# Kernel tuning notes

Hardware: AMD Instinct MI355X
Metric: run time of the kernel (lower is better)

## Reference

```python
import jax, jax.numpy as jnp
from jax import lax
import numpy as np

HIDDEN = 64
E = 2.0        # SigmaLayer E
E_INFTY = 0.5  # SigmaLayer E_infty


def _glorot(key, shape):
    fan_in, fan_out = shape
    lim = np.sqrt(6.0 / (fan_in + fan_out)).astype(np.float32)
    return jax.random.uniform(key, shape, jnp.float32, -lim, lim)


def setup_inputs() -> dict:
    key = jax.random.key(0)
    ks = jax.random.split(key, 7)
    B, T = 2048, 1024
    x = jax.random.uniform(ks[0], (B, T, 2), jnp.float32)  # [:, :, 0]=eps, [:, :, 1]=dt (>0)
    W1 = _glorot(ks[1], (2, HIDDEN))
    b1 = jnp.zeros((HIDDEN,), jnp.float32)
    W2 = _glorot(ks[2], (HIDDEN, HIDDEN))
    b2 = jnp.zeros((HIDDEN,), jnp.float32)
    W3 = _glorot(ks[3], (HIDDEN, 1))
    b3 = jnp.zeros((1,), jnp.float32)
    return {"x": x, "W1": W1, "b1": b1, "W2": W2, "b2": b2, "W3": W3, "b3": b3}


def reference(x, W1, b1, W2, b2, W3, b3):
    # x: [B, T, 2] -> sigma: [B, T, 1]
    def step(gamma, xt):  # gamma: [B,1], xt: [B,2]
        eps_n = xt[:, :1]
        dt_n = xt[:, 1:2]
        h = jnp.concatenate([eps_n, gamma], axis=-1)      # [B,2]
        h = jnp.tanh(h @ W1 + b1)                         # [B,H]
        h = jnp.tanh(h @ W2 + b2)                         # [B,H]
        gamma_dot = h @ W3 + b3                           # [B,1]
        gamma_new = gamma + dt_n * gamma_dot              # explicit Euler
        return gamma_new, gamma_new

    B = x.shape[0]
    g0 = jnp.zeros((B, 1), x.dtype)
    _, gammas = lax.scan(step, g0, jnp.swapaxes(x, 0, 1))  # [T,B,1]
    gamma = jnp.swapaxes(gammas, 0, 1)                     # [B,T,1]
    eps = x[:, :, :1]
    sigma = E_INFTY * eps + E * (eps - gamma)
    return sigma
```

## Files before the change

### kernel.cpp

```cpp
#include <hip/hip_runtime.h>


typedef float f2 __attribute__((ext_vector_type(2)));
typedef float f4 __attribute__((ext_vector_type(4)));

__device__ __forceinline__ float tanh_fast(float x) {
    float e = __builtin_amdgcn_exp2f(x * 2.885390081777927f);
    float r = __builtin_amdgcn_rcpf(e + 1.0f);
    return fmaf(-2.0f, r, 1.0f);
}

template<int CTRL>
__device__ __forceinline__ float dpp_add(float v) {
    int m = __builtin_amdgcn_update_dpp(0, __float_as_int(v), CTRL, 0xF, 0xF, true);
    return v + __int_as_float(m);
}

__device__ __forceinline__ float quad_sum(float v) {
    v = dpp_add<0xB1>(v);
    v = dpp_add<0x4E>(v);
    return v;
}

__device__ __forceinline__ float wave_sum_bcast(float v) {
    v = dpp_add<0xB1>(v);
    v = dpp_add<0x4E>(v);
    v = dpp_add<0x141>(v);
    v = dpp_add<0x140>(v);
    v = dpp_add<0x142>(v);
    v = dpp_add<0x143>(v);
    return __int_as_float(__builtin_amdgcn_readlane(__float_as_int(v), 63));
}

__device__ __forceinline__ float rl(float v, int k) {
    return __int_as_float(__builtin_amdgcn_readlane(__float_as_int(v), k));
}

__global__ __attribute__((amdgpu_flat_work_group_size(256, 256),
                          amdgpu_waves_per_eu(2, 2)))
void maxwell_scan_kernel(
    const float* __restrict__ x,  const float* __restrict__ W1,
    const float* __restrict__ b1, const float* __restrict__ W2,
    const float* __restrict__ b2, const float* __restrict__ W3,
    const float* __restrict__ b3, float* __restrict__ out)
{
    __shared__ __align__(16) float lds_h1[4][64];
    const int lane = threadIdx.x & 63;
    const int warp = threadIdx.x >> 6;
    const int b    = (blockIdx.x << 2) + warp;

    const int o = lane >> 2;
    const int k = lane & 3;
    const int jsel = o + 16 * k;

    const float w1_0 = W1[lane];
    const float w1_1 = W1[64 + lane];
    const float b1j  = b1[lane];
    const float b2s  = b2[jsel];
    const float w3s  = W3[jsel];
    const float b3s  = b3[0];

    f2 w2r[4][8];
#pragma unroll
    for (int m = 0; m < 4; ++m) {
#pragma unroll
        for (int p = 0; p < 8; ++p) {
            const int i0 = 16 * k + 2 * p;
            const int j  = o + 16 * m;
            w2r[m][p] = (f2){ W2[i0 * 64 + j], W2[(i0 + 1) * 64 + j] };
        }
    }

    float* h1s = lds_h1[warp];
    const f4* hv = (const f4*)h1s + (k << 2);

    const f2* __restrict__ xrow = (const f2*)(x) + (size_t)b * 1024;
    float*    __restrict__ orow = out + (size_t)b * 1024;

    float gamma = 0.0f;
    f2 vx = xrow[lane];

    for (int c = 0; c < 16; ++c) {
        f2 vx_next = vx;
        if (c < 15) vx_next = xrow[(c + 1) * 64 + lane];
        float vsig = 0.0f;

        for (int s = 0; s < 8; ++s) {
            const int k0 = s * 8;
            float pk[8], dtk[8], sg[8];
#pragma unroll
            for (int t = 0; t < 8; ++t) {
                const float e = rl(vx.x, k0 + t);
                dtk[t] = rl(vx.y, k0 + t);
                pk[t]  = fmaf(e, w1_0, b1j);
                sg[t]  = 2.5f * e;
            }

            asm volatile("" : "+v"(w2r[0][0]), "+v"(w2r[0][1]), "+v"(w2r[0][2]), "+v"(w2r[0][3]),
                              "+v"(w2r[0][4]), "+v"(w2r[0][5]), "+v"(w2r[0][6]), "+v"(w2r[0][7]),
                              "+v"(w2r[1][0]), "+v"(w2r[1][1]), "+v"(w2r[1][2]), "+v"(w2r[1][3]),
                              "+v"(w2r[1][4]), "+v"(w2r[1][5]), "+v"(w2r[1][6]), "+v"(w2r[1][7]));
            asm volatile("" : "+v"(w2r[2][0]), "+v"(w2r[2][1]), "+v"(w2r[2][2]), "+v"(w2r[2][3]),
                              "+v"(w2r[2][4]), "+v"(w2r[2][5]), "+v"(w2r[2][6]), "+v"(w2r[2][7]),
                              "+v"(w2r[3][0]), "+v"(w2r[3][1]), "+v"(w2r[3][2]), "+v"(w2r[3][3]),
                              "+v"(w2r[3][4]), "+v"(w2r[3][5]), "+v"(w2r[3][6]), "+v"(w2r[3][7]));

#pragma unroll
            for (int t = 0; t < 8; ++t) {
                const float h1 = tanh_fast(fmaf(gamma, w1_1, pk[t]));
                h1s[lane] = h1;
                __builtin_amdgcn_wave_barrier();

                f2 a0 = {0.f, 0.f}, a1 = {0.f, 0.f}, a2 = {0.f, 0.f}, a3 = {0.f, 0.f};
#pragma unroll
                for (int q = 0; q < 4; ++q) {
                    const f4 h4 = hv[q];
                    const f2 hlo = (f2){h4.x, h4.y};
                    const f2 hhi = (f2){h4.z, h4.w};
                    a0 += hlo * w2r[0][2 * q];  a0 += hhi * w2r[0][2 * q + 1];
                    a1 += hlo * w2r[1][2 * q];  a1 += hhi * w2r[1][2 * q + 1];
                    a2 += hlo * w2r[2][2 * q];  a2 += hhi * w2r[2][2 * q + 1];
                    a3 += hlo * w2r[3][2 * q];  a3 += hhi * w2r[3][2 * q + 1];
                }
                __builtin_amdgcn_wave_barrier();

                float s0 = quad_sum(a0.x + a0.y);
                float s1 = quad_sum(a1.x + a1.y);
                float s2 = quad_sum(a2.x + a2.y);
                float s3 = quad_sum(a3.x + a3.y);
                const float t01 = (k & 1) ? s1 : s0;
                const float t23 = (k & 1) ? s3 : s2;
                const float pre = (k & 2) ? t23 : t01;
                const float h2 = tanh_fast(pre + b2s);

                const float gdot = wave_sum_bcast(h2 * w3s) + b3s;
                gamma = fmaf(dtk[t], gdot, gamma);

                const float sig = fmaf(-2.0f, gamma, sg[t]);
                vsig = (lane == k0 + t) ? sig : vsig;
            }
        }
        orow[c * 64 + lane] = vsig;
        vx = vx_next;
    }
}

extern "C" void kernel_launch(void* const* d_in, const int* in_sizes, int n_in,
                              void* d_out, int out_size, void* d_ws, size_t ws_size,
                              hipStream_t stream) {
    const float* x  = (const float*)d_in[0];
    const float* W1 = (const float*)d_in[1];
    const float* b1 = (const float*)d_in[2];
    const float* W2 = (const float*)d_in[3];
    const float* b2 = (const float*)d_in[4];
    const float* W3 = (const float*)d_in[5];
    const float* b3 = (const float*)d_in[6];
    float* out = (float*)d_out;
    (void)in_sizes; (void)n_in; (void)d_ws; (void)ws_size; (void)out_size;

    maxwell_scan_kernel<<<512, 256, 0, stream>>>(x, W1, b1, W2, b2, W3, b3, out);
}
```

Measured before the change: 420.9 us.

## Use fp16 dot2 with ds_bpermute for hidden layer, fold tanh affine terms

Replaces the LDS store/load exchange of h1 with DPP plus ds_bpermute of packed fp16 pairs, and computes the 64x64 layer with v_dot2 fp16 instructions. The affine part of tanh (1 - 2r) is folded into prescaled weights and biases, so each tanh reduces to exp and rcp. The goal is to shorten the per-timestep serial dependency chain and halve the FMA count. The cost is fp16 precision on h1 and W2 inside a 1024-step recurrence, which may drift from the reference.

```diff
diff --git a/kernel.cpp b/kernel.cpp
--- a/kernel.cpp
+++ b/kernel.cpp
@@ -2,13 +2,9 @@
 
 
 typedef float f2 __attribute__((ext_vector_type(2)));
-typedef float f4 __attribute__((ext_vector_type(4)));
+typedef _Float16 h2v __attribute__((ext_vector_type(2)));
 
-__device__ __forceinline__ float tanh_fast(float x) {
-    float e = __builtin_amdgcn_exp2f(x * 2.885390081777927f);
-    float r = __builtin_amdgcn_rcpf(e + 1.0f);
-    return fmaf(-2.0f, r, 1.0f);
-}
+#define TANH_C 2.885390081777927f
 
 template<int CTRL>
 __device__ __forceinline__ float dpp_add(float v) {
@@ -44,7 +40,6 @@
     const float* __restrict__ b2, const float* __restrict__ W3,
     const float* __restrict__ b3, float* __restrict__ out)
 {
-    __shared__ __align__(16) float lds_h1[4][64];
     const int lane = threadIdx.x & 63;
     const int warp = threadIdx.x >> 6;
     const int b    = (blockIdx.x << 2) + warp;
@@ -56,23 +51,32 @@
     const float w1_0 = W1[lane];
     const float w1_1 = W1[64 + lane];
     const float b1j  = b1[lane];
-    const float b2s  = b2[jsel];
-    const float w3s  = W3[jsel];
-    const float b3s  = b3[0];
 
-    f2 w2r[4][8];
+    const float w3p = -2.0f * W3[jsel];
+    float sW3 = 0.0f;
+    for (int j = 0; j < 64; ++j) sW3 += W3[j];
+    const float b3p = b3[0] + sW3;
+
+    int   w2h[4][8];
+    float b2q[4];
 #pragma unroll
     for (int m = 0; m < 4; ++m) {
+        const int j = o + 16 * m;
+        float cs = 0.0f;
+        for (int i = 0; i < 64; ++i) cs += (float)(_Float16)W2[i * 64 + j];
+        b2q[m] = 0.25f * (b2[j] + cs);
 #pragma unroll
         for (int p = 0; p < 8; ++p) {
             const int i0 = 16 * k + 2 * p;
-            const int j  = o + 16 * m;
-            w2r[m][p] = (f2){ W2[i0 * 64 + j], W2[(i0 + 1) * 64 + j] };
+            h2v pp = { (_Float16)(-2.0f * W2[i0 * 64 + j]),
+                       (_Float16)(-2.0f * W2[(i0 + 1) * 64 + j]) };
+            w2h[m][p] = __builtin_bit_cast(int, pp);
         }
     }
 
-    float* h1s = lds_h1[warp];
-    const f4* hv = (const f4*)h1s + (k << 2);
+    int baddr[8];
+#pragma unroll
+    for (int p = 0; p < 8; ++p) baddr[p] = (16 * k + 2 * p) << 2;
 
     const f2* __restrict__ xrow = (const f2*)(x) + (size_t)b * 1024;
     float*    __restrict__ orow = out + (size_t)b * 1024;
@@ -87,54 +91,78 @@
 
         for (int s = 0; s < 8; ++s) {
             const int k0 = s * 8;
-            float pk[8], dtk[8], sg[8];
+            float pk[8], dtk[8], sg[8], db3[8];
 #pragma unroll
             for (int t = 0; t < 8; ++t) {
                 const float e = rl(vx.x, k0 + t);
                 dtk[t] = rl(vx.y, k0 + t);
                 pk[t]  = fmaf(e, w1_0, b1j);
                 sg[t]  = 2.5f * e;
+                db3[t] = dtk[t] * b3p;
             }
 
-            asm volatile("" : "+v"(w2r[0][0]), "+v"(w2r[0][1]), "+v"(w2r[0][2]), "+v"(w2r[0][3]),
-                              "+v"(w2r[0][4]), "+v"(w2r[0][5]), "+v"(w2r[0][6]), "+v"(w2r[0][7]),
-                              "+v"(w2r[1][0]), "+v"(w2r[1][1]), "+v"(w2r[1][2]), "+v"(w2r[1][3]),
-                              "+v"(w2r[1][4]), "+v"(w2r[1][5]), "+v"(w2r[1][6]), "+v"(w2r[1][7]));
-            asm volatile("" : "+v"(w2r[2][0]), "+v"(w2r[2][1]), "+v"(w2r[2][2]), "+v"(w2r[2][3]),
-                              "+v"(w2r[2][4]), "+v"(w2r[2][5]), "+v"(w2r[2][6]), "+v"(w2r[2][7]),
-                              "+v"(w2r[3][0]), "+v"(w2r[3][1]), "+v"(w2r[3][2]), "+v"(w2r[3][3]),
-                              "+v"(w2r[3][4]), "+v"(w2r[3][5]), "+v"(w2r[3][6]), "+v"(w2r[3][7]));
+            asm volatile("" : "+v"(w2h[0][0]), "+v"(w2h[0][1]), "+v"(w2h[0][2]), "+v"(w2h[0][3]),
+                              "+v"(w2h[0][4]), "+v"(w2h[0][5]), "+v"(w2h[0][6]), "+v"(w2h[0][7]),
+                              "+v"(w2h[1][0]), "+v"(w2h[1][1]), "+v"(w2h[1][2]), "+v"(w2h[1][3]),
+                              "+v"(w2h[1][4]), "+v"(w2h[1][5]), "+v"(w2h[1][6]), "+v"(w2h[1][7]));
+            asm volatile("" : "+v"(w2h[2][0]), "+v"(w2h[2][1]), "+v"(w2h[2][2]), "+v"(w2h[2][3]),
+                              "+v"(w2h[2][4]), "+v"(w2h[2][5]), "+v"(w2h[2][6]), "+v"(w2h[2][7]),
+                              "+v"(w2h[3][0]), "+v"(w2h[3][1]), "+v"(w2h[3][2]), "+v"(w2h[3][3]),
+                              "+v"(w2h[3][4]), "+v"(w2h[3][5]), "+v"(w2h[3][6]), "+v"(w2h[3][7]));
 
 #pragma unroll
             for (int t = 0; t < 8; ++t) {
-                const float h1 = tanh_fast(fmaf(gamma, w1_1, pk[t]));
-                h1s[lane] = h1;
-                __builtin_amdgcn_wave_barrier();
+                const float a  = fmaf(gamma, w1_1, pk[t]);
+                const float ea = __builtin_amdgcn_exp2f(a * TANH_C);
+                const float r  = __builtin_amdgcn_rcpf(ea + 1.0f);
 
-                f2 a0 = {0.f, 0.f}, a1 = {0.f, 0.f}, a2 = {0.f, 0.f}, a3 = {0.f, 0.f};
+                const int nb = __builtin_amdgcn_update_dpp(
+                    0, __float_as_int(r), 0x101, 0xF, 0xF, true);
+                const int packd = __builtin_bit_cast(
+                    int, __builtin_amdgcn_cvt_pkrtz(r, __int_as_float(nb)));
+
+                int w0 = __builtin_amdgcn_ds_bpermute(baddr[0], packd);
+                int w1 = __builtin_amdgcn_ds_bpermute(baddr[1], packd);
+                int w2 = __builtin_amdgcn_ds_bpermute(baddr[2], packd);
+                int w3 = __builtin_amdgcn_ds_bpermute(baddr[3], packd);
+                int w4 = __builtin_amdgcn_ds_bpermute(baddr[4], packd);
+                int w5 = __builtin_amdgcn_ds_bpermute(baddr[5], packd);
+                int w6 = __builtin_amdgcn_ds_bpermute(baddr[6], packd);
+                int w7 = __builtin_amdgcn_ds_bpermute(baddr[7], packd);
+
+                const float gpre = gamma + db3[t];
+
+                float zacc[4];
 #pragma unroll
-                for (int q = 0; q < 4; ++q) {
-                    const f4 h4 = hv[q];
-                    const f2 hlo = (f2){h4.x, h4.y};
-                    const f2 hhi = (f2){h4.z, h4.w};
-                    a0 += hlo * w2r[0][2 * q];  a0 += hhi * w2r[0][2 * q + 1];
-                    a1 += hlo * w2r[1][2 * q];  a1 += hhi * w2r[1][2 * q + 1];
-                    a2 += hlo * w2r[2][2 * q];  a2 += hhi * w2r[2][2 * q + 1];
-                    a3 += hlo * w2r[3][2 * q];  a3 += hhi * w2r[3][2 * q + 1];
+                for (int m = 0; m < 4; ++m) {
+                    float aA = b2q[m], aB = 0.0f;
+                    aA = __builtin_amdgcn_fdot2(__builtin_bit_cast(h2v, w2h[m][0]),
+                                                __builtin_bit_cast(h2v, w0), aA, false);
+                    aB = __builtin_amdgcn_fdot2(__builtin_bit_cast(h2v, w2h[m][4]),
+                                                __builtin_bit_cast(h2v, w4), aB, false);
+                    aA = __builtin_amdgcn_fdot2(__builtin_bit_cast(h2v, w2h[m][1]),
+                                                __builtin_bit_cast(h2v, w1), aA, false);
+                    aB = __builtin_amdgcn_fdot2(__builtin_bit_cast(h2v, w2h[m][5]),
+                                                __builtin_bit_cast(h2v, w5), aB, false);
+                    aA = __builtin_amdgcn_fdot2(__builtin_bit_cast(h2v, w2h[m][2]),
+                                                __builtin_bit_cast(h2v, w2), aA, false);
+                    aB = __builtin_amdgcn_fdot2(__builtin_bit_cast(h2v, w2h[m][6]),
+                                                __builtin_bit_cast(h2v, w6), aB, false);
+                    aA = __builtin_amdgcn_fdot2(__builtin_bit_cast(h2v, w2h[m][3]),
+                                                __builtin_bit_cast(h2v, w3), aA, false);
+                    aB = __builtin_amdgcn_fdot2(__builtin_bit_cast(h2v, w2h[m][7]),
+                                                __builtin_bit_cast(h2v, w7), aB, false);
+                    zacc[m] = quad_sum(aA + aB);
                 }
-                __builtin_amdgcn_wave_barrier();
 
-                float s0 = quad_sum(a0.x + a0.y);
-                float s1 = quad_sum(a1.x + a1.y);
-                float s2 = quad_sum(a2.x + a2.y);
-                float s3 = quad_sum(a3.x + a3.y);
-                const float t01 = (k & 1) ? s1 : s0;
-                const float t23 = (k & 1) ? s3 : s2;
-                const float pre = (k & 2) ? t23 : t01;
-                const float h2 = tanh_fast(pre + b2s);
+                const float t01 = (k & 1) ? zacc[1] : zacc[0];
+                const float t23 = (k & 1) ? zacc[3] : zacc[2];
+                const float z   = (k & 2) ? t23 : t01;
 
-                const float gdot = wave_sum_bcast(h2 * w3s) + b3s;
-                gamma = fmaf(dtk[t], gdot, gamma);
+                const float e2 = __builtin_amdgcn_exp2f(z * TANH_C);
+                const float r2 = __builtin_amdgcn_rcpf(e2 + 1.0f);
+                const float ws = wave_sum_bcast(r2 * w3p);
+                gamma = fmaf(dtk[t], ws, gpre);
 
                 const float sig = fmaf(-2.0f, gamma, sg[t]);
                 vsig = (lane == k0 + t) ? sig : vsig;
```

New measurement: 450.6 us. 1.07x slower.
